# Kernel optimization log

Measured on AMD Instinct MI355X. Metric: run time of the kernel, lower is better.

Reference implementation:

```python
import jax, jax.numpy as jnp
import numpy as np

D_MODEL = 1024
NUM_HEADS = 16
HEAD_DIM = D_MODEL // NUM_HEADS


def setup_inputs() -> dict:
    key = jax.random.key(0)
    ks = jax.random.split(key, 5)
    x = jax.random.normal(ks[0], (2, 2048, D_MODEL), dtype=jnp.float32)
    s = 1.0 / np.sqrt(D_MODEL)
    # nn.Linear weight is [out, in]; y = x @ W.T
    Wq = jax.random.normal(ks[1], (D_MODEL, D_MODEL), dtype=jnp.float32) * s
    Wk = jax.random.normal(ks[2], (D_MODEL, D_MODEL), dtype=jnp.float32) * s
    Wv = jax.random.normal(ks[3], (D_MODEL, D_MODEL), dtype=jnp.float32) * s
    Wo = jax.random.normal(ks[4], (D_MODEL, D_MODEL), dtype=jnp.float32) * s
    return {"x": x, "Wq": Wq, "Wk": Wk, "Wv": Wv, "Wo": Wo}


def reference(x, Wq, Wk, Wv, Wo):
    b, s, d = x.shape
    h, hd = NUM_HEADS, HEAD_DIM
    # projections (Linear: x @ W.T), reshape to [b, h, s, hd]
    def proj(W):
        return (x @ W.T).reshape(b, s, h, hd).transpose(0, 2, 1, 3)
    Q, K, V = proj(Wq), proj(Wk), proj(Wv)
    # NOTE: original scales by 1/sqrt(d_model), not 1/sqrt(head_dim)
    scores = jnp.einsum('bhqd,bhkd->bhqk', Q, K) / jnp.sqrt(jnp.float32(d))
    attn = jax.nn.softmax(scores, axis=-1)
    ctx = jnp.einsum('bhqk,bhkd->bhqd', attn, V)
    ctx = ctx.transpose(0, 2, 1, 3).reshape(b, s, d)
    return ctx @ Wo.T
```

## Files before the change

kernel.cpp:

```cpp
#include <hip/hip_runtime.h>
#include <cstddef>
#include <cstdint>

#define SEQ 2048
#define DM 1024
#define NH 16
#define HD 64

typedef _Float16 f16;
typedef __attribute__((ext_vector_type(8))) _Float16 f16x8;
typedef __attribute__((ext_vector_type(4))) _Float16 f16x4;
typedef __attribute__((ext_vector_type(2))) _Float16 f16x2;
typedef __attribute__((ext_vector_type(4))) float f32x4;

__global__ __launch_bounds__(256) void cast_all(const float* __restrict__ x,
                                                const float* __restrict__ Wq,
                                                const float* __restrict__ Wk,
                                                const float* __restrict__ Wv,
                                                const float* __restrict__ Wo,
                                                f16* __restrict__ dst) {
  const int i = blockIdx.x * 256 + threadIdx.x;
  const float* src;
  int off;
  if (i < 1048576) {
    src = x; off = i;
  } else {
    const int j = i - 1048576;
    const int wsel = j >> 18;
    src = (wsel == 0) ? Wq : (wsel == 1) ? Wk : (wsel == 2) ? Wv : Wo;
    off = j & 262143;
  }
  const float4 v = ((const float4*)src)[off];
  f16x4 o = {(f16)v.x, (f16)v.y, (f16)v.z, (f16)v.w};
  ((f16x4*)dst)[i] = o;
}

__device__ __forceinline__ void gload16(const void* g, void* lds) {
  __builtin_amdgcn_global_load_lds((const __attribute__((address_space(1))) void*)g,
                                   (__attribute__((address_space(3))) void*)lds,
                                   16, 0, 0);
}

__device__ __forceinline__ void gemm_tile(const f16* __restrict__ A,
                                          const f16* __restrict__ B,
                                          f16* As, f16* Bs,
                                          int K, f32x4 acc[4][4]) {
  const int t = threadIdx.x;
  const int lane = t & 63;
  const int w = t >> 6;
  const int wm = (w & 1) << 6, wn = (w >> 1) << 6;
  const int srow = lane >> 2, scol = lane & 3;
  const int fr = lane & 15, q = lane >> 4;
  for (int k0 = 0; k0 < K; k0 += 32) {
    __syncthreads();
#pragma unroll
    for (int c = 0; c < 2; ++c) {
      const int chunk = (w << 1) + c;
      const int row = (chunk << 4) + srow;
      gload16(A + (size_t)row * K + k0 + (scol << 3), As + (chunk << 9));
      gload16(B + (size_t)row * K + k0 + (scol << 3), Bs + (chunk << 9));
    }
    __syncthreads();
    f16x8 af[4], bfr[4];
#pragma unroll
    for (int i = 0; i < 4; ++i)
      af[i] = *(const f16x8*)(As + (wm + (i << 4) + fr) * 32 + (q << 3));
#pragma unroll
    for (int j = 0; j < 4; ++j)
      bfr[j] = *(const f16x8*)(Bs + (wn + (j << 4) + fr) * 32 + (q << 3));
#pragma unroll
    for (int i = 0; i < 4; ++i)
#pragma unroll
      for (int j = 0; j < 4; ++j)
        acc[i][j] = __builtin_amdgcn_mfma_f32_16x16x32_f16(af[i], bfr[j],
                                                           acc[i][j], 0, 0, 0);
  }
}

#define QSCALE 0.04508422003f
__global__ __launch_bounds__(256) void gemm_qkv(
    const f16* __restrict__ xb, const f16* __restrict__ Wqb,
    const f16* __restrict__ Wkb, const f16* __restrict__ Wvb,
    f16* __restrict__ Qb, f16* __restrict__ Kb, f16* __restrict__ Vtg) {
  __shared__ f16 smem[16896];
  f16* As = smem;
  f16* Bs = smem + 4096;
  const int which = blockIdx.x >> 3;
  const int bn = (blockIdx.x & 7) << 7;
  const int bm = blockIdx.y << 7;
  const f16* B = (which == 0) ? Wqb : (which == 1) ? Wkb : Wvb;
  f32x4 acc[4][4] = {};
  gemm_tile(xb + (size_t)bm * DM, B + (size_t)bn * DM, As, Bs, DM, acc);
  const int t = threadIdx.x;
  const int lane = t & 63, w = t >> 6;
  const int wm = (w & 1) << 6, wn = (w >> 1) << 6;
  const int col = lane & 15, q = lane >> 4;
  if (which < 2) {
    f16* C = (which == 0) ? Qb : Kb;
    const float sc = (which == 0) ? QSCALE : 1.0f;
    __syncthreads();
#pragma unroll
    for (int i = 0; i < 4; ++i) {
      const int m0 = wm + (i << 4) + (q << 2);
#pragma unroll
      for (int j = 0; j < 4; ++j) {
        const int n = wn + (j << 4) + col;
#pragma unroll
        for (int r = 0; r < 4; ++r)
          smem[(m0 + r) * 132 + n] = (f16)(acc[i][j][r] * sc);
      }
    }
    __syncthreads();
#pragma unroll
    for (int p = 0; p < 8; ++p) {
      const int idx = t + (p << 8);
      const int row = idx >> 4, c8 = (idx & 15) << 3;
      const f16x8 v = *(const f16x8*)(smem + row * 132 + c8);
      *(f16x8*)(C + (size_t)(bm + row) * DM + bn + c8) = v;
    }
  } else {
    const int b = bm >> 11, sb = bm & 2047;
#pragma unroll
    for (int i = 0; i < 4; ++i) {
      const int sg = sb + wm + (i << 4) + (q << 2);
#pragma unroll
      for (int j = 0; j < 4; ++j) {
        const int n = bn + wn + (j << 4) + col;
        const int bh = (b << 4) + (n >> 6), d = n & 63;
        f16x4 o = {(f16)acc[i][j][0], (f16)acc[i][j][1],
                   (f16)acc[i][j][2], (f16)acc[i][j][3]};
        const size_t flat = ((size_t)bh << 17) + ((size_t)(sg >> 6) << 12) +
                            (((sg >> 2) & 15) << 8) + (d << 2);
        *(f16x4*)(Vtg + flat) = o;
      }
    }
  }
}

__global__ __launch_bounds__(256) void gemm_out(const f16* __restrict__ Ab,
                                                const f16* __restrict__ Wob,
                                                float* __restrict__ out) {
  __shared__ f16 As[128 * 32];
  __shared__ f16 Bs[128 * 32];
  const int bn = blockIdx.x << 7, bm = blockIdx.y << 7;
  f32x4 acc[4][4] = {};
  gemm_tile(Ab + (size_t)bm * DM, Wob + (size_t)bn * DM, As, Bs, DM, acc);
  const int lane = threadIdx.x & 63, w = threadIdx.x >> 6;
  const int wm = (w & 1) << 6, wn = (w >> 1) << 6;
  const int col = lane & 15, q = lane >> 4;
#pragma unroll
  for (int i = 0; i < 4; ++i) {
    const int m = bm + wm + (i << 4) + (q << 2);
#pragma unroll
    for (int j = 0; j < 4; ++j) {
      const int n = bn + wn + (j << 4) + col;
#pragma unroll
      for (int r = 0; r < 4; ++r)
        out[(size_t)(m + r) * DM + n] = acc[i][j][r];
    }
  }
}

__global__ __launch_bounds__(256, 2) void attn_mfma(const f16* __restrict__ Qb,
                                                    const f16* __restrict__ Kb,
                                                    const f16* __restrict__ Vtg,
                                                    f16* __restrict__ Ctx) {
  __shared__ f16 smem[8192];
  const int t = threadIdx.x, lane = t & 63, w = t >> 6;
  const int fr = lane & 15, quad = lane >> 4;
  const int i = blockIdx.x;
  const int j = i >> 3;
  const int bh = ((i & 7) << 2) + (j >> 4);
  const int qt16 = j & 15;
  const int b = bh >> 4, h = bh & 15;

  const size_t qrow0 = (size_t)b * SEQ + qt16 * 128 + w * 32;

  f16x8 Qf[2][2];
#pragma unroll
  for (int qt = 0; qt < 2; ++qt)
#pragma unroll
    for (int hf = 0; hf < 2; ++hf)
      Qf[qt][hf] = *(const f16x8*)(Qb + (qrow0 + qt * 16 + fr) * DM + h * HD +
                                   hf * 32 + (quad << 3));

  const int krow = lane >> 2, kkc = lane & 3;
  const f16* Kg = Kb + ((size_t)b * SEQ + 16 * w + krow) * DM + h * HD + (kkc << 3);
  const int cwr = ((krow >> 1) << 3) | ((krow & 1) << 2) | (((krow >> 1) + kkc) & 3);
  const int wofs = (w << 9) + (cwr << 3);
  const int crd = ((fr >> 1) << 3) | ((fr & 1) << 2) | (((fr >> 1) + quad) & 3);

  const f16* Vg = Vtg + ((size_t)bh << 17) + (quad << 8) + (fr << 2);

  f16x8 kreg[2];
  f16x4 va[4][4], vb[4][4];
  auto loadK = [&](int kt) {
#pragma unroll
    for (int hf = 0; hf < 2; ++hf)
      kreg[hf] = *(const f16x8*)(Kg + (size_t)kt * 64 * DM + hf * 32);
  };
  auto loadV = [&](int kt, f16x4 (&vr)[4][4]) {
#pragma unroll
    for (int kc = 0; kc < 4; ++kc)
#pragma unroll
      for (int dt = 0; dt < 4; ++dt)
        vr[dt][kc] = *(const f16x4*)(Vg + kt * 4096 + (kc << 10) + (dt << 6));
  };

  f32x4 acc[2][4] = {};
  float lacc[2] = {0.f, 0.f};

  f16* img0 = smem;
  f16* img1 = smem + 4096;

  loadK(0);
  loadV(0, va);
  *(f16x8*)(img0 + wofs) = kreg[0];
  *(f16x8*)(img0 + wofs + 2048) = kreg[1];

  auto body = [&](int kt, f16x4 (&vcur)[4][4], f16x4 (&vnxt)[4][4],
                  f16* imgR, f16* imgW) {
    __syncthreads();
    if (kt < 31) {
      loadK(kt + 1);
      loadV(kt + 1, vnxt);
    }
    f16x8 Kf[4][2];
#pragma unroll
    for (int mt = 0; mt < 4; ++mt)
#pragma unroll
      for (int hf = 0; hf < 2; ++hf)
        Kf[mt][hf] = *(const f16x8*)(imgR + (crd << 3) + hf * 2048 + (mt << 9));

    f16x4 pf[2][4];
#pragma unroll
    for (int qt = 0; qt < 2; ++qt) {
      f32x4 z[4] = {};
#pragma unroll
      for (int mt = 0; mt < 4; ++mt) {
        z[mt] = __builtin_amdgcn_mfma_f32_16x16x32_f16(Kf[mt][0], Qf[qt][0],
                                                       z[mt], 0, 0, 0);
        z[mt] = __builtin_amdgcn_mfma_f32_16x16x32_f16(Kf[mt][1], Qf[qt][1],
                                                       z[mt], 0, 0, 0);
      }
#pragma unroll
      for (int mt = 0; mt < 4; ++mt) {
        const float p0 = __builtin_amdgcn_exp2f(z[mt][0]);
        const float p1 = __builtin_amdgcn_exp2f(z[mt][1]);
        const float p2 = __builtin_amdgcn_exp2f(z[mt][2]);
        const float p3 = __builtin_amdgcn_exp2f(z[mt][3]);
        lacc[qt] += (p0 + p1) + (p2 + p3);
        const f16x2 lo = __builtin_bit_cast(f16x2, __builtin_amdgcn_cvt_pkrtz(p0, p1));
        const f16x2 hi = __builtin_bit_cast(f16x2, __builtin_amdgcn_cvt_pkrtz(p2, p3));
        f16x4 pv; pv.x = lo.x; pv.y = lo.y; pv.z = hi.x; pv.w = hi.y;
        pf[qt][mt] = pv;
      }
    }

#pragma unroll
    for (int dt = 0; dt < 4; ++dt)
#pragma unroll
      for (int kc = 0; kc < 4; ++kc)
#pragma unroll
        for (int qt = 0; qt < 2; ++qt)
          acc[qt][dt] = __builtin_amdgcn_mfma_f32_16x16x16f16(vcur[dt][kc],
                                                              pf[qt][kc],
                                                              acc[qt][dt], 0, 0, 0);
    if (kt < 31) {
      *(f16x8*)(imgW + wofs) = kreg[0];
      *(f16x8*)(imgW + wofs + 2048) = kreg[1];
    }
  };

  for (int kt = 0; kt < 32; kt += 2) {
    body(kt, va, vb, img0, img1);
    body(kt + 1, vb, va, img1, img0);
  }

  float inv[2];
#pragma unroll
  for (int qt = 0; qt < 2; ++qt) {
    float l = lacc[qt];
    l += __shfl_xor(l, 16);
    l += __shfl_xor(l, 32);
    inv[qt] = __builtin_amdgcn_rcpf(l);
  }

  __syncthreads();
  f16* T = smem + (w << 11);
#pragma unroll
  for (int qt = 0; qt < 2; ++qt)
#pragma unroll
    for (int dt = 0; dt < 4; ++dt) {
      f16x4 o = {(f16)(acc[qt][dt][0] * inv[qt]), (f16)(acc[qt][dt][1] * inv[qt]),
                 (f16)(acc[qt][dt][2] * inv[qt]), (f16)(acc[qt][dt][3] * inv[qt])};
      *(f16x4*)(T + (qt * 16 + fr) * 64 + dt * 16 + (quad << 2)) = o;
    }
#pragma unroll
  for (int p = 0; p < 4; ++p) {
    const int ql = p * 8 + (lane >> 3);
    const f16x8 v = *(const f16x8*)(T + ql * 64 + ((lane & 7) << 3));
    *(f16x8*)(Ctx + (qrow0 + ql) * DM + h * HD + ((lane & 7) << 3)) = v;
  }
}

extern "C" void kernel_launch(void* const* d_in, const int* in_sizes, int n_in,
                              void* d_out, int out_size, void* d_ws, size_t ws_size,
                              hipStream_t stream) {
  const float* x  = (const float*)d_in[0];
  const float* Wq = (const float*)d_in[1];
  const float* Wk = (const float*)d_in[2];
  const float* Wv = (const float*)d_in[3];
  const float* Wo = (const float*)d_in[4];

  char* ws = (char*)d_ws;
  f16* xb  = (f16*)(ws);
  f16* Wb  = (f16*)(ws + (8u << 20));
  f16* Wqb = Wb;
  f16* Wkb = Wb + 1048576;
  f16* Wvb = Wb + 2097152;
  f16* Wob = Wb + 3145728;
  f16* Qb  = (f16*)(ws + (16u << 20));
  f16* Kb  = (f16*)(ws + (24u << 20));
  f16* Vtg = (f16*)(ws + (32u << 20));
  f16* Ctx = (f16*)(ws + (40u << 20));

  cast_all<<<8192, 256, 0, stream>>>(x, Wq, Wk, Wv, Wo, xb);

  gemm_qkv<<<dim3(24, 32), 256, 0, stream>>>(xb, Wqb, Wkb, Wvb, Qb, Kb, Vtg);
  attn_mfma<<<dim3(2 * NH * (SEQ / 128)), 256, 0, stream>>>(Qb, Kb, Vtg, Ctx);
  gemm_out<<<dim3(8, 32), 256, 0, stream>>>(Ctx, Wob, (float*)d_out);
}
```

Baseline: 193.4 us.

## Halve attention query tile and output GEMM N-tile to double grid sizes

The attention kernel now gives each block 64 query rows (16 per wave) instead of 128, which doubles the grid to 1024 blocks and raises the occupancy hint to 4 blocks per CU. The output projection GEMM moves from 128x128 to 128x64 tiles with its own inline load loop, doubling its grid to 512 blocks. The aim is better CU fill on a GPU with many CUs. The cost is that each K/V tile loaded into shared memory or registers is reused by half as many query rows, so attention global traffic roughly doubles, and the GEMM loses some arithmetic intensity.

```diff
diff --git a/kernel.cpp b/kernel.cpp
--- a/kernel.cpp
+++ b/kernel.cpp
@@ -140,19 +140,47 @@
 __global__ __launch_bounds__(256) void gemm_out(const f16* __restrict__ Ab,
                                                 const f16* __restrict__ Wob,
                                                 float* __restrict__ out) {
-  __shared__ f16 As[128 * 32];
-  __shared__ f16 Bs[128 * 32];
-  const int bn = blockIdx.x << 7, bm = blockIdx.y << 7;
-  f32x4 acc[4][4] = {};
-  gemm_tile(Ab + (size_t)bm * DM, Wob + (size_t)bn * DM, As, Bs, DM, acc);
-  const int lane = threadIdx.x & 63, w = threadIdx.x >> 6;
-  const int wm = (w & 1) << 6, wn = (w >> 1) << 6;
-  const int col = lane & 15, q = lane >> 4;
+  __shared__ f16 As[4096];
+  __shared__ f16 Bs[2048];
+  const int bn = blockIdx.x << 6, bm = blockIdx.y << 7;
+  const int t = threadIdx.x, lane = t & 63, w = t >> 6;
+  const int wm = (w & 1) << 6, wn = (w >> 1) << 5;
+  const int srow = lane >> 2, scol = lane & 3;
+  const int fr = lane & 15, q = lane >> 4;
+  f32x4 acc[4][2] = {};
+  for (int k0 = 0; k0 < DM; k0 += 32) {
+    __syncthreads();
+#pragma unroll
+    for (int c = 0; c < 2; ++c) {
+      const int chunk = (w << 1) + c;
+      const int row = (chunk << 4) + srow;
+      gload16(Ab + (size_t)(bm + row) * DM + k0 + (scol << 3), As + (chunk << 9));
+    }
+    {
+      const int row = (w << 4) + srow;
+      gload16(Wob + (size_t)(bn + row) * DM + k0 + (scol << 3), Bs + (w << 9));
+    }
+    __syncthreads();
+    f16x8 af[4], bfr[2];
+#pragma unroll
+    for (int i = 0; i < 4; ++i)
+      af[i] = *(const f16x8*)(As + (wm + (i << 4) + fr) * 32 + (q << 3));
+#pragma unroll
+    for (int j = 0; j < 2; ++j)
+      bfr[j] = *(const f16x8*)(Bs + (wn + (j << 4) + fr) * 32 + (q << 3));
+#pragma unroll
+    for (int i = 0; i < 4; ++i)
+#pragma unroll
+      for (int j = 0; j < 2; ++j)
+        acc[i][j] = __builtin_amdgcn_mfma_f32_16x16x32_f16(af[i], bfr[j],
+                                                           acc[i][j], 0, 0, 0);
+  }
+  const int col = lane & 15;
 #pragma unroll
   for (int i = 0; i < 4; ++i) {
     const int m = bm + wm + (i << 4) + (q << 2);
 #pragma unroll
-    for (int j = 0; j < 4; ++j) {
+    for (int j = 0; j < 2; ++j) {
       const int n = bn + wn + (j << 4) + col;
 #pragma unroll
       for (int r = 0; r < 4; ++r)
@@ -161,7 +189,7 @@
   }
 }
 
-__global__ __launch_bounds__(256, 2) void attn_mfma(const f16* __restrict__ Qb,
+__global__ __launch_bounds__(256, 4) void attn_mfma(const f16* __restrict__ Qb,
                                                     const f16* __restrict__ Kb,
                                                     const f16* __restrict__ Vtg,
                                                     f16* __restrict__ Ctx) {
@@ -170,19 +198,17 @@
   const int fr = lane & 15, quad = lane >> 4;
   const int i = blockIdx.x;
   const int j = i >> 3;
-  const int bh = ((i & 7) << 2) + (j >> 4);
-  const int qt16 = j & 15;
+  const int bh = ((i & 7) << 2) + (j >> 5);
+  const int qt = j & 31;
   const int b = bh >> 4, h = bh & 15;
 
-  const size_t qrow0 = (size_t)b * SEQ + qt16 * 128 + w * 32;
-
-  f16x8 Qf[2][2];
-#pragma unroll
-  for (int qt = 0; qt < 2; ++qt)
-#pragma unroll
-    for (int hf = 0; hf < 2; ++hf)
-      Qf[qt][hf] = *(const f16x8*)(Qb + (qrow0 + qt * 16 + fr) * DM + h * HD +
-                                   hf * 32 + (quad << 3));
+  const size_t qrow0 = (size_t)b * SEQ + qt * 64 + w * 16;
+
+  f16x8 Qf[2];
+#pragma unroll
+  for (int hf = 0; hf < 2; ++hf)
+    Qf[hf] = *(const f16x8*)(Qb + (qrow0 + fr) * DM + h * HD + hf * 32 +
+                             (quad << 3));
 
   const int krow = lane >> 2, kkc = lane & 3;
   const f16* Kg = Kb + ((size_t)b * SEQ + 16 * w + krow) * DM + h * HD + (kkc << 3);
@@ -207,8 +233,8 @@
         vr[dt][kc] = *(const f16x4*)(Vg + kt * 4096 + (kc << 10) + (dt << 6));
   };
 
-  f32x4 acc[2][4] = {};
-  float lacc[2] = {0.f, 0.f};
+  f32x4 acc[4] = {};
+  float lacc = 0.f;
 
   f16* img0 = smem;
   f16* img1 = smem + 4096;
@@ -232,40 +258,34 @@
       for (int hf = 0; hf < 2; ++hf)
         Kf[mt][hf] = *(const f16x8*)(imgR + (crd << 3) + hf * 2048 + (mt << 9));
 
-    f16x4 pf[2][4];
-#pragma unroll
-    for (int qt = 0; qt < 2; ++qt) {
-      f32x4 z[4] = {};
-#pragma unroll
-      for (int mt = 0; mt < 4; ++mt) {
-        z[mt] = __builtin_amdgcn_mfma_f32_16x16x32_f16(Kf[mt][0], Qf[qt][0],
-                                                       z[mt], 0, 0, 0);
-        z[mt] = __builtin_amdgcn_mfma_f32_16x16x32_f16(Kf[mt][1], Qf[qt][1],
-                                                       z[mt], 0, 0, 0);
-      }
-#pragma unroll
-      for (int mt = 0; mt < 4; ++mt) {
-        const float p0 = __builtin_amdgcn_exp2f(z[mt][0]);
-        const float p1 = __builtin_amdgcn_exp2f(z[mt][1]);
-        const float p2 = __builtin_amdgcn_exp2f(z[mt][2]);
-        const float p3 = __builtin_amdgcn_exp2f(z[mt][3]);
-        lacc[qt] += (p0 + p1) + (p2 + p3);
-        const f16x2 lo = __builtin_bit_cast(f16x2, __builtin_amdgcn_cvt_pkrtz(p0, p1));
-        const f16x2 hi = __builtin_bit_cast(f16x2, __builtin_amdgcn_cvt_pkrtz(p2, p3));
-        f16x4 pv; pv.x = lo.x; pv.y = lo.y; pv.z = hi.x; pv.w = hi.y;
-        pf[qt][mt] = pv;
-      }
+    f32x4 z[4] = {};
+#pragma unroll
+    for (int mt = 0; mt < 4; ++mt) {
+      z[mt] = __builtin_amdgcn_mfma_f32_16x16x32_f16(Kf[mt][0], Qf[0], z[mt],
+                                                     0, 0, 0);
+      z[mt] = __builtin_amdgcn_mfma_f32_16x16x32_f16(Kf[mt][1], Qf[1], z[mt],
+                                                     0, 0, 0);
+    }
+    f16x4 pf[4];
+#pragma unroll
+    for (int mt = 0; mt < 4; ++mt) {
+      const float p0 = __builtin_amdgcn_exp2f(z[mt][0]);
+      const float p1 = __builtin_amdgcn_exp2f(z[mt][1]);
+      const float p2 = __builtin_amdgcn_exp2f(z[mt][2]);
+      const float p3 = __builtin_amdgcn_exp2f(z[mt][3]);
+      lacc += (p0 + p1) + (p2 + p3);
+      const f16x2 lo = __builtin_bit_cast(f16x2, __builtin_amdgcn_cvt_pkrtz(p0, p1));
+      const f16x2 hi = __builtin_bit_cast(f16x2, __builtin_amdgcn_cvt_pkrtz(p2, p3));
+      f16x4 pv; pv.x = lo.x; pv.y = lo.y; pv.z = hi.x; pv.w = hi.y;
+      pf[mt] = pv;
     }
 
 #pragma unroll
     for (int dt = 0; dt < 4; ++dt)
 #pragma unroll
       for (int kc = 0; kc < 4; ++kc)
-#pragma unroll
-        for (int qt = 0; qt < 2; ++qt)
-          acc[qt][dt] = __builtin_amdgcn_mfma_f32_16x16x16f16(vcur[dt][kc],
-                                                              pf[qt][kc],
-                                                              acc[qt][dt], 0, 0, 0);
+        acc[dt] = __builtin_amdgcn_mfma_f32_16x16x16f16(vcur[dt][kc], pf[kc],
+                                                        acc[dt], 0, 0, 0);
     if (kt < 31) {
       *(f16x8*)(imgW + wofs) = kreg[0];
       *(f16x8*)(imgW + wofs + 2048) = kreg[1];
@@ -277,27 +297,21 @@
     body(kt + 1, vb, va, img1, img0);
   }
 
-  float inv[2];
-#pragma unroll
-  for (int qt = 0; qt < 2; ++qt) {
-    float l = lacc[qt];
-    l += __shfl_xor(l, 16);
-    l += __shfl_xor(l, 32);
-    inv[qt] = __builtin_amdgcn_rcpf(l);
-  }
+  float l = lacc;
+  l += __shfl_xor(l, 16);
+  l += __shfl_xor(l, 32);
+  const float inv = __builtin_amdgcn_rcpf(l);
 
   __syncthreads();
-  f16* T = smem + (w << 11);
-#pragma unroll
-  for (int qt = 0; qt < 2; ++qt)
-#pragma unroll
-    for (int dt = 0; dt < 4; ++dt) {
-      f16x4 o = {(f16)(acc[qt][dt][0] * inv[qt]), (f16)(acc[qt][dt][1] * inv[qt]),
-                 (f16)(acc[qt][dt][2] * inv[qt]), (f16)(acc[qt][dt][3] * inv[qt])};
-      *(f16x4*)(T + (qt * 16 + fr) * 64 + dt * 16 + (quad << 2)) = o;
-    }
-#pragma unroll
-  for (int p = 0; p < 4; ++p) {
+  f16* T = smem + (w << 10);
+#pragma unroll
+  for (int dt = 0; dt < 4; ++dt) {
+    f16x4 o = {(f16)(acc[dt][0] * inv), (f16)(acc[dt][1] * inv),
+               (f16)(acc[dt][2] * inv), (f16)(acc[dt][3] * inv)};
+    *(f16x4*)(T + fr * 64 + dt * 16 + (quad << 2)) = o;
+  }
+#pragma unroll
+  for (int p = 0; p < 2; ++p) {
     const int ql = p * 8 + (lane >> 3);
     const f16x8 v = *(const f16x8*)(T + ql * 64 + ((lane & 7) << 3));
     *(f16x8*)(Ctx + (qrow0 + ql) * DM + h * HD + ((lane & 7) << 3)) = v;
@@ -328,6 +342,6 @@
   cast_all<<<8192, 256, 0, stream>>>(x, Wq, Wk, Wv, Wo, xb);
 
   gemm_qkv<<<dim3(24, 32), 256, 0, stream>>>(xb, Wqb, Wkb, Wvb, Qb, Kb, Vtg);
-  attn_mfma<<<dim3(2 * NH * (SEQ / 128)), 256, 0, stream>>>(Qb, Kb, Vtg, Ctx);
-  gemm_out<<<dim3(8, 32), 256, 0, stream>>>(Ctx, Wob, (float*)d_out);
-}
+  attn_mfma<<<dim3(2 * NH * (SEQ / 64)), 256, 0, stream>>>(Qb, Kb, Vtg, Ctx);
+  gemm_out<<<dim3(16, 32), 256, 0, stream>>>(Ctx, Wob, (float*)d_out);
+}
```

After: 288.8 us. +49.3%, slower.

## Split attention KV range in two with a combine pass, and retile the output GEMM

Applied to the files above, without the earlier changes.

The attention kernel now splits each head's key/value sequence into two halves, processed by separate blocks. The grid doubles to 1024 blocks, and each block writes a normalized partial context plus its row sums. A new combine kernel merges the two halves by their softmax mass. This is exact here because no running max is subtracted. The output GEMM switches to 128x64 tiles with an inline single-buffered loop, doubling its block count to improve CU fill. In exchange, the split adds an extra kernel launch and extra global traffic for the partial outputs, and the `__launch_bounds__` occupancy hint is dropped from the attention kernel.

```diff
diff --git a/kernel.cpp b/kernel.cpp
--- a/kernel.cpp
+++ b/kernel.cpp
@@ -140,19 +140,47 @@
 __global__ __launch_bounds__(256) void gemm_out(const f16* __restrict__ Ab,
                                                 const f16* __restrict__ Wob,
                                                 float* __restrict__ out) {
-  __shared__ f16 As[128 * 32];
-  __shared__ f16 Bs[128 * 32];
-  const int bn = blockIdx.x << 7, bm = blockIdx.y << 7;
-  f32x4 acc[4][4] = {};
-  gemm_tile(Ab + (size_t)bm * DM, Wob + (size_t)bn * DM, As, Bs, DM, acc);
-  const int lane = threadIdx.x & 63, w = threadIdx.x >> 6;
-  const int wm = (w & 1) << 6, wn = (w >> 1) << 6;
-  const int col = lane & 15, q = lane >> 4;
+  __shared__ f16 As[4096];
+  __shared__ f16 Bs[2048];
+  const int bn = blockIdx.x << 6, bm = blockIdx.y << 7;
+  const int t = threadIdx.x, lane = t & 63, w = t >> 6;
+  const int wm = (w & 1) << 6, wn = (w >> 1) << 5;
+  const int srow = lane >> 2, scol = lane & 3;
+  const int fr = lane & 15, q = lane >> 4;
+  f32x4 acc[4][2] = {};
+  for (int k0 = 0; k0 < DM; k0 += 32) {
+    __syncthreads();
+#pragma unroll
+    for (int c = 0; c < 2; ++c) {
+      const int chunk = (w << 1) + c;
+      const int row = (chunk << 4) + srow;
+      gload16(Ab + (size_t)(bm + row) * DM + k0 + (scol << 3), As + (chunk << 9));
+    }
+    {
+      const int row = (w << 4) + srow;
+      gload16(Wob + (size_t)(bn + row) * DM + k0 + (scol << 3), Bs + (w << 9));
+    }
+    __syncthreads();
+    f16x8 af[4], bfr[2];
+#pragma unroll
+    for (int i = 0; i < 4; ++i)
+      af[i] = *(const f16x8*)(As + (wm + (i << 4) + fr) * 32 + (q << 3));
+#pragma unroll
+    for (int j = 0; j < 2; ++j)
+      bfr[j] = *(const f16x8*)(Bs + (wn + (j << 4) + fr) * 32 + (q << 3));
+#pragma unroll
+    for (int i = 0; i < 4; ++i)
+#pragma unroll
+      for (int j = 0; j < 2; ++j)
+        acc[i][j] = __builtin_amdgcn_mfma_f32_16x16x32_f16(af[i], bfr[j],
+                                                           acc[i][j], 0, 0, 0);
+  }
+  const int col = lane & 15;
 #pragma unroll
   for (int i = 0; i < 4; ++i) {
     const int m = bm + wm + (i << 4) + (q << 2);
 #pragma unroll
-    for (int j = 0; j < 4; ++j) {
+    for (int j = 0; j < 2; ++j) {
       const int n = bn + wn + (j << 4) + col;
 #pragma unroll
       for (int r = 0; r < 4; ++r)
@@ -161,18 +189,24 @@
   }
 }
 
-__global__ __launch_bounds__(256, 2) void attn_mfma(const f16* __restrict__ Qb,
-                                                    const f16* __restrict__ Kb,
-                                                    const f16* __restrict__ Vtg,
-                                                    f16* __restrict__ Ctx) {
+__global__ __launch_bounds__(256) void attn_mfma(const f16* __restrict__ Qb,
+                                                 const f16* __restrict__ Kb,
+                                                 const f16* __restrict__ Vtg,
+                                                 f16* __restrict__ Po0,
+                                                 f16* __restrict__ Po1,
+                                                 float* __restrict__ Pl0,
+                                                 float* __restrict__ Pl1) {
   __shared__ f16 smem[8192];
   const int t = threadIdx.x, lane = t & 63, w = t >> 6;
   const int fr = lane & 15, quad = lane >> 4;
   const int i = blockIdx.x;
   const int j = i >> 3;
-  const int bh = ((i & 7) << 2) + (j >> 4);
-  const int qt16 = j & 15;
+  const int bh = ((i & 7) << 2) + (j >> 5);
+  const int rem = j & 31;
+  const int sp = rem >> 4;
+  const int qt16 = rem & 15;
   const int b = bh >> 4, h = bh & 15;
+  const int kbeg = sp << 4;
 
   const size_t qrow0 = (size_t)b * SEQ + qt16 * 128 + w * 32;
 
@@ -213,17 +247,17 @@
   f16* img0 = smem;
   f16* img1 = smem + 4096;
 
-  loadK(0);
-  loadV(0, va);
+  loadK(kbeg);
+  loadV(kbeg, va);
   *(f16x8*)(img0 + wofs) = kreg[0];
   *(f16x8*)(img0 + wofs + 2048) = kreg[1];
 
-  auto body = [&](int kt, f16x4 (&vcur)[4][4], f16x4 (&vnxt)[4][4],
+  auto body = [&](int n, f16x4 (&vcur)[4][4], f16x4 (&vnxt)[4][4],
                   f16* imgR, f16* imgW) {
     __syncthreads();
-    if (kt < 31) {
-      loadK(kt + 1);
-      loadV(kt + 1, vnxt);
+    if (n < 15) {
+      loadK(kbeg + n + 1);
+      loadV(kbeg + n + 1, vnxt);
     }
     f16x8 Kf[4][2];
 #pragma unroll
@@ -266,24 +300,35 @@
           acc[qt][dt] = __builtin_amdgcn_mfma_f32_16x16x16f16(vcur[dt][kc],
                                                               pf[qt][kc],
                                                               acc[qt][dt], 0, 0, 0);
-    if (kt < 31) {
+    if (n < 15) {
       *(f16x8*)(imgW + wofs) = kreg[0];
       *(f16x8*)(imgW + wofs + 2048) = kreg[1];
     }
   };
 
-  for (int kt = 0; kt < 32; kt += 2) {
-    body(kt, va, vb, img0, img1);
-    body(kt + 1, vb, va, img1, img0);
-  }
-
-  float inv[2];
+  for (int n = 0; n < 16; n += 2) {
+    body(n, va, vb, img0, img1);
+    body(n + 1, vb, va, img1, img0);
+  }
+
+  float lsum[2], inv[2];
 #pragma unroll
   for (int qt = 0; qt < 2; ++qt) {
     float l = lacc[qt];
     l += __shfl_xor(l, 16);
     l += __shfl_xor(l, 32);
+    lsum[qt] = l;
     inv[qt] = __builtin_amdgcn_rcpf(l);
+  }
+
+  f16* Po = sp ? Po1 : Po0;
+  float* Pl = sp ? Pl1 : Pl0;
+  const size_t pbase = ((size_t)(bh * 16 + qt16) * 128);
+
+  if (quad == 0) {
+#pragma unroll
+    for (int qt = 0; qt < 2; ++qt)
+      Pl[pbase + w * 32 + qt * 16 + fr] = lsum[qt];
   }
 
   __syncthreads();
@@ -300,8 +345,32 @@
   for (int p = 0; p < 4; ++p) {
     const int ql = p * 8 + (lane >> 3);
     const f16x8 v = *(const f16x8*)(T + ql * 64 + ((lane & 7) << 3));
-    *(f16x8*)(Ctx + (qrow0 + ql) * DM + h * HD + ((lane & 7) << 3)) = v;
-  }
+    *(f16x8*)(Po + (pbase + w * 32 + ql) * 64 + ((lane & 7) << 3)) = v;
+  }
+}
+
+__global__ __launch_bounds__(256) void attn_combine(
+    const f16* __restrict__ Po0, const f16* __restrict__ Po1,
+    const float* __restrict__ Pl0, const float* __restrict__ Pl1,
+    f16* __restrict__ Ctx) {
+  const int idx = blockIdx.x * 256 + threadIdx.x;
+  const int m = idx >> 7, g = idx & 127;
+  const int b = m >> 11, s = m & 2047;
+  const int h = g >> 3;
+  const int bh = (b << 4) + h;
+  const int qt = s >> 7, q = s & 127;
+  const size_t po = ((size_t)(bh * 16 + qt) * 128 + q) * 64 + ((g & 7) << 3);
+  const int pl = (bh * 16 + qt) * 128 + q;
+  const f16x8 o0 = *(const f16x8*)(Po0 + po);
+  const f16x8 o1 = *(const f16x8*)(Po1 + po);
+  const float l0 = Pl0[pl], l1 = Pl1[pl];
+  const float inv = __builtin_amdgcn_rcpf(l0 + l1);
+  const float w0 = l0 * inv, w1 = l1 * inv;
+  f16x8 r;
+#pragma unroll
+  for (int j = 0; j < 8; ++j)
+    r[j] = (f16)(w0 * (float)o0[j] + w1 * (float)o1[j]);
+  *(f16x8*)(Ctx + (size_t)m * DM + (size_t)g * 8) = r;
 }
 
 extern "C" void kernel_launch(void* const* d_in, const int* in_sizes, int n_in,
@@ -323,11 +392,16 @@
   f16* Qb  = (f16*)(ws + (16u << 20));
   f16* Kb  = (f16*)(ws + (24u << 20));
   f16* Vtg = (f16*)(ws + (32u << 20));
-  f16* Ctx = (f16*)(ws + (40u << 20));
+  f16*   Po0 = (f16*)(ws);
+  f16*   Po1 = (f16*)(ws + (40u << 20));
+  float* Pl0 = (float*)(ws + (8u << 20));
+  float* Pl1 = (float*)(ws + (8u << 20) + (256u << 10));
+  f16*   Ctx = (f16*)(ws + (48u << 20));
 
   cast_all<<<8192, 256, 0, stream>>>(x, Wq, Wk, Wv, Wo, xb);
 
   gemm_qkv<<<dim3(24, 32), 256, 0, stream>>>(xb, Wqb, Wkb, Wvb, Qb, Kb, Vtg);
-  attn_mfma<<<dim3(2 * NH * (SEQ / 128)), 256, 0, stream>>>(Qb, Kb, Vtg, Ctx);
-  gemm_out<<<dim3(8, 32), 256, 0, stream>>>(Ctx, Wob, (float*)d_out);
-}
+  attn_mfma<<<dim3(1024), 256, 0, stream>>>(Qb, Kb, Vtg, Po0, Po1, Pl0, Pl1);
+  attn_combine<<<dim3(2048), 256, 0, stream>>>(Po0, Po1, Pl0, Pl1, Ctx);
+  gemm_out<<<dim3(16, 32), 256, 0, stream>>>(Ctx, Wob, (float*)d_out);
+}
```

Measured after the change: 197.7 us. 1.02x slower.
